# Kernel optimization log

Hardware: AMD Instinct MI355X
Metric: run time of the kernel (lower is better)

## Reference

```python
import jax, jax.numpy as jnp
import numpy as np
from jax import lax

ALPHA = 50.0
BN_EPS = 1e-5
L2_EPS = 1e-12

N, C, H, W = 32, 128, 128, 128
K = 64  # num_clusters


def _l2norm(v, axis):
    n = jnp.sqrt(jnp.sum(v * v, axis=axis, keepdims=True))
    return v / jnp.maximum(n, L2_EPS)


def setup_inputs() -> dict:
    key = jax.random.key(0)
    ks = jax.random.split(key, 4)
    x = jax.random.normal(ks[0], (N, C, H, W), dtype=jnp.float32)
    conv_w = jax.random.normal(ks[1], (C, C, 3, 3), dtype=jnp.float32) * 0.05
    bn_gamma = jnp.ones((C,), jnp.float32)
    bn_beta = jnp.zeros((C,), jnp.float32)
    bn_mean = jnp.zeros((C,), jnp.float32)
    bn_var = jnp.ones((C,), jnp.float32)
    # conv.weight in NetVLAD is centroids.permute(1,0): shape (dim, num_clusters)
    vlad_w = jax.random.normal(ks[2], (C, K), dtype=jnp.float32)
    vlad_b = jnp.zeros((K,), jnp.float32)  # initialized to zeros in _init_params
    return {"input": x, "conv_w": conv_w, "bn_gamma": bn_gamma, "bn_beta": bn_beta,
            "bn_mean": bn_mean, "bn_var": bn_var, "vlad_w": vlad_w, "vlad_b": vlad_b,
            "norm_flag": 1}


def reference(input, conv_w, bn_gamma, bn_beta, bn_mean, bn_var, vlad_w, vlad_b, norm_flag):
    # bottleneck_layer_2: conv3x3 stride2 pad1 (no bias) -> BN (eval form) -> ReLU
    f = lax.conv_general_dilated(input, conv_w, window_strides=(2, 2),
                                 padding=[(1, 1), (1, 1)],
                                 dimension_numbers=("NCHW", "OIHW", "NCHW"))
    inv = bn_gamma / jnp.sqrt(bn_var + BN_EPS)
    f = f * inv[None, :, None, None] + (bn_beta - bn_mean * inv)[None, :, None, None]
    f = jax.nn.relu(f)

    n, c, h, w = f.shape
    hw = h * w
    # normalize_input: L2 over channel dim
    xn = _l2norm(f, axis=1)
    xf = xn.reshape(n, c, hw)  # (N,C,HW)

    # soft assignment: x^T @ normalize(W, dim=0), bias added, softmax over clusters
    wn = _l2norm(vlad_w, axis=0)                     # (C,K)
    sa_ = jnp.einsum("nci,ck->nik", xf, wn)          # (N,HW,K)
    logits = jnp.swapaxes(sa_, 1, 2) + vlad_b[None, :, None]  # (N,K,HW)
    a = jax.nn.softmax(ALPHA * logits, axis=1)       # softmax over K

    # vlad_k = sum_i a_ki * x_i - (sum_i a_ki) * c_k  (c_k = vlad_w[:,k], unnormalized)
    asum = jnp.sum(a, axis=-1)                       # (N,K)
    vlad = jnp.einsum("nki,nci->nkc", a, xf) - asum[:, :, None] * vlad_w.T[None]  # (N,K,C)

    vlad = _l2norm(vlad, axis=2)                     # intra-normalization
    vlad = vlad.reshape(n, -1)
    vlad = _l2norm(vlad, axis=1)

    feature = jnp.swapaxes(xf, 1, 2)                 # (N,HW,C)
    soft_assign_out = jnp.swapaxes(sa_, 1, 2)        # (N,K,HW)
    return (vlad, soft_assign_out, feature)
```

## Files before the change

### kernel.cpp

```cpp
#include <hip/hip_runtime.h>

typedef short short8 __attribute__((ext_vector_type(8)));
typedef float floatx4 __attribute__((ext_vector_type(4)));

#define ALPHA 50.0f
#define BN_EPS 1e-5f

#define SA_BASE   262144L
#define FEAT_BASE 8650752L

#define T_OFF    0L
#define AW_OFF   0L
#define XNT_OFF  138444800L
#define WB_OFF   171999232L
#define WNA_OFF  172294144L
#define ASUM_OFF 172310528L

__device__ __forceinline__ unsigned short f2bf(float f) {
    unsigned u = __builtin_bit_cast(unsigned, f);
    u = u + 0x7FFFu + ((u >> 16) & 1u);
    return (unsigned short)(u >> 16);
}

__global__ __launch_bounds__(256) void k_prep(const float* __restrict__ conv_w,
                                              const float* __restrict__ vlad_w,
                                              unsigned short* __restrict__ wB,
                                              unsigned short* __restrict__ wnA,
                                              float* __restrict__ asum) {
    int b = blockIdx.x, t = threadIdx.x;
    if (b < 576) {
        int idx = b * 256 + t;
        int ci = idx & 127, co = (idx >> 7) & 127, tap = idx >> 14;
        float w = conv_w[(co * 128 + ci) * 9 + tap];
        wB[(tap * 128 + co) * 128 + ci] = f2bf(w);
    } else {
        if (t < 64) {
            int k = t;
            float s = 0.0f;
            for (int c = 0; c < 128; c++) { float w = vlad_w[c * 64 + k]; s += w * w; }
            float rs = 1.0f / fmaxf(sqrtf(s), 1e-12f);
            for (int c = 0; c < 128; c++) wnA[k * 128 + c] = f2bf(vlad_w[c * 64 + k] * rs);
        } else {
            for (int i = t - 64; i < 2048; i += 192) asum[i] = 0.0f;
        }
    }
}

__global__ __launch_bounds__(256) void k_border(unsigned short* __restrict__ T) {
    int n = blockIdx.x, t = threadIdx.x;
    uint4 z = make_uint4(0, 0, 0, 0);
    for (int i = t; i < 4128; i += 256) {
        long e;
        if (i < 2080) {
            int ix = i >> 4, oct = i & 15;
            e = (((long)n * 130 + 0) * 130 + ix) * 128 + oct * 8;
        } else {
            int j = i - 2080;
            int row = (j >> 4) + 1, oct = j & 15;
            e = (((long)n * 130 + row) * 130 + 0) * 128 + oct * 8;
        }
        *(uint4*)(T + e) = z;
    }
}

__global__ __launch_bounds__(256) void k_xform(const float* __restrict__ in,
                                               unsigned short* __restrict__ T) {
    int y = blockIdx.x, n = blockIdx.y, t = threadIdx.x;
    __shared__ float ls[32 * 132];
    for (int cc = 0; cc < 4; cc++) {
        __syncthreads();
        int ci0 = cc * 32;
        for (int i = 0; i < 4; i++) {
            int idx = i * 256 + t;
            int ci = idx >> 5, xq = idx & 31;
            float4 v = *(const float4*)(in + ((((long)n * 128 + ci0 + ci) * 128 + y) * 128 + xq * 4));
            *(float4*)(&ls[ci * 132 + xq * 4]) = v;
        }
        __syncthreads();
        int x = t >> 1, half = t & 1;
        for (int o = 0; o < 2; o++) {
            short8 pk;
#pragma unroll
            for (int j = 0; j < 8; j++) {
                int lci = half * 16 + o * 8 + j;
                pk[j] = (short)f2bf(ls[lci * 132 + x]);
            }
            long e = (((long)n * 130 + y + 1) * 130 + (x + 1)) * 128 + ci0 + half * 16 + o * 8;
            *(short8*)(T + e) = pk;
        }
    }
}

__global__ __launch_bounds__(256) void k_conv(const unsigned short* __restrict__ T,
                                              const unsigned short* __restrict__ wB,
                                              const float* __restrict__ gamma,
                                              const float* __restrict__ beta,
                                              const float* __restrict__ mean,
                                              const float* __restrict__ var,
                                              float* __restrict__ out,
                                              unsigned short* __restrict__ xnT) {
    int ypair = blockIdx.x, n = blockIdx.y;
    int t = threadIdx.x, lane = t & 63, w = t >> 6;
    int wm = w >> 1, wn = w & 1;
    int s = lane & 15, q = lane >> 4;
    int y0 = ypair * 2;

    __shared__ short lsA[26000];
    __shared__ float lsq[256];

    floatx4 acc[4][4];
#pragma unroll
    for (int a = 0; a < 4; a++)
#pragma unroll
        for (int b = 0; b < 4; b++) acc[a][b] = (floatx4){0.f, 0.f, 0.f, 0.f};

    const unsigned short* Tbase = T + (((long)n * 130 + 2 * y0) * 130) * 128;

    int abase0 = 10400 * wm + q * 8;
    int bbase0 = (wn * 64 + s) * 128 + q * 8;

    for (int cc = 0; cc < 4; cc++) {
        int ci0 = cc * 32;
        for (int i = 0; i < 11; i++) {
            int idx = i * 256 + t;
            if (idx < 2600) {
                int oct = idx & 3, rem = idx >> 2;
                int ix = rem % 130, r = rem / 130;
                uint4 v = *(const uint4*)(Tbase + (long)(r * 130 + ix) * 128 + ci0 + oct * 8);
                *(uint4*)(&lsA[(r * 130 + ix) * 40 + oct * 8]) = v;
            }
        }
        __syncthreads();
#pragma unroll
        for (int tap = 0; tap < 9; tap++) {
            int dy = tap / 3, dx = tap % 3;
            short8 af[4], bf[4];
#pragma unroll
            for (int tm = 0; tm < 4; tm++) {
                int x = tm * 16 + s;
                af[tm] = *(const short8*)(&lsA[abase0 + 80 * x + 5200 * dy + 40 * dx]);
            }
#pragma unroll
            for (int tn = 0; tn < 4; tn++) {
                bf[tn] = *(const short8*)(wB + bbase0 + tap * 16384 + tn * 2048 + ci0);
            }
#pragma unroll
            for (int tm = 0; tm < 4; tm++)
#pragma unroll
                for (int tn = 0; tn < 4; tn++)
                    acc[tm][tn] = __builtin_amdgcn_mfma_f32_16x16x32_bf16(af[tm], bf[tn], acc[tm][tn], 0, 0, 0);
        }
        __syncthreads();
    }

    float inv[4], bt[4];
#pragma unroll
    for (int tn = 0; tn < 4; tn++) {
        int co = wn * 64 + tn * 16 + s;
        inv[tn] = gamma[co] / sqrtf(var[co] + BN_EPS);
        bt[tn] = beta[co] - mean[co] * inv[tn];
    }
#pragma unroll
    for (int tm = 0; tm < 4; tm++)
#pragma unroll
        for (int tn = 0; tn < 4; tn++)
#pragma unroll
            for (int r = 0; r < 4; r++) {
                float f = acc[tm][tn][r] * inv[tn] + bt[tn];
                acc[tm][tn][r] = fmaxf(f, 0.0f);
            }
#pragma unroll
    for (int tm = 0; tm < 4; tm++)
#pragma unroll
        for (int r = 0; r < 4; r++) {
            float p = 0.f;
#pragma unroll
            for (int tn = 0; tn < 4; tn++) { float f = acc[tm][tn][r]; p += f * f; }
            p += __shfl_xor(p, 1); p += __shfl_xor(p, 2);
            p += __shfl_xor(p, 4); p += __shfl_xor(p, 8);
            if (s == 0) lsq[wn * 128 + wm * 64 + tm * 16 + q * 4 + r] = p;
        }
    __syncthreads();
    float scl[4][4];
#pragma unroll
    for (int tm = 0; tm < 4; tm++)
#pragma unroll
        for (int r = 0; r < 4; r++) {
            int m = wm * 64 + tm * 16 + q * 4 + r;
            float tot = lsq[m] + lsq[128 + m];
            scl[tm][r] = 1.0f / fmaxf(sqrtf(tot), 1e-12f);
        }
    short* lsT = lsA;
    long pixbase = (long)n * 4096 + y0 * 64;
#pragma unroll
    for (int tm = 0; tm < 4; tm++)
#pragma unroll
        for (int r = 0; r < 4; r++) {
            int m = wm * 64 + tm * 16 + q * 4 + r;
#pragma unroll
            for (int tn = 0; tn < 4; tn++) {
                int co = wn * 64 + tn * 16 + s;
                float xv = acc[tm][tn][r] * scl[tm][r];
                out[FEAT_BASE + (pixbase + m) * 128 + co] = xv;
                lsT[co * 136 + m] = (short)f2bf(xv);
            }
        }
    __syncthreads();
    {
        int co = t >> 1, mh = t & 1;
        long base = ((long)n * 128 + co) * 4096 + y0 * 64 + mh * 64;
#pragma unroll
        for (int o = 0; o < 8; o++) {
            short8 v = *(short8*)(&lsT[co * 136 + mh * 64 + o * 8]);
            *(short8*)(xnT + base + o * 8) = v;
        }
    }
}

__global__ __launch_bounds__(256) void k_sa(const float* __restrict__ feat,
                                            const unsigned short* __restrict__ wnA,
                                            const float* __restrict__ vlad_b,
                                            float* __restrict__ out,
                                            unsigned short* __restrict__ aout,
                                            float* __restrict__ asum) {
    int pt = blockIdx.x, n = blockIdx.y;
    int t = threadIdx.x, lane = t & 63, w = t >> 6;
    int s = lane & 15, q = lane >> 4;
    int pb = pt * 256 + w * 64;

    floatx4 acc[4][4];
#pragma unroll
    for (int a = 0; a < 4; a++)
#pragma unroll
        for (int b = 0; b < 4; b++) acc[a][b] = (floatx4){0.f, 0.f, 0.f, 0.f};

    const float* fb = feat + FEAT_BASE + (long)n * 4096 * 128;
#pragma unroll
    for (int kk = 0; kk < 4; kk++) {
        int c0 = kk * 32 + q * 8;
        short8 af[4], bf[4];
#pragma unroll
        for (int tm = 0; tm < 4; tm++)
            af[tm] = *(const short8*)(wnA + (tm * 16 + s) * 128 + c0);
#pragma unroll
        for (int tn = 0; tn < 4; tn++) {
            const float* p = fb + (long)(pb + tn * 16 + s) * 128 + c0;
            float4 v0 = *(const float4*)p;
            float4 v1 = *(const float4*)(p + 4);
            short8 bv;
            bv[0] = (short)f2bf(v0.x); bv[1] = (short)f2bf(v0.y);
            bv[2] = (short)f2bf(v0.z); bv[3] = (short)f2bf(v0.w);
            bv[4] = (short)f2bf(v1.x); bv[5] = (short)f2bf(v1.y);
            bv[6] = (short)f2bf(v1.z); bv[7] = (short)f2bf(v1.w);
            bf[tn] = bv;
        }
#pragma unroll
        for (int tm = 0; tm < 4; tm++)
#pragma unroll
            for (int tn = 0; tn < 4; tn++)
                acc[tm][tn] = __builtin_amdgcn_mfma_f32_16x16x32_bf16(af[tm], bf[tn], acc[tm][tn], 0, 0, 0);
    }
    long sabase = SA_BASE + (long)n * 64 * 4096;
#pragma unroll
    for (int tm = 0; tm < 4; tm++)
#pragma unroll
        for (int r = 0; r < 4; r++) {
            int k = tm * 16 + q * 4 + r;
#pragma unroll
            for (int tn = 0; tn < 4; tn++)
                out[sabase + (long)k * 4096 + pb + tn * 16 + s] = acc[tm][tn][r];
        }
    float bv[4][4];
#pragma unroll
    for (int tm = 0; tm < 4; tm++)
#pragma unroll
        for (int r = 0; r < 4; r++) bv[tm][r] = vlad_b[tm * 16 + q * 4 + r];
#pragma unroll
    for (int tn = 0; tn < 4; tn++) {
        float M = -1e30f;
#pragma unroll
        for (int tm = 0; tm < 4; tm++)
#pragma unroll
            for (int r = 0; r < 4; r++)
                M = fmaxf(M, ALPHA * (acc[tm][tn][r] + bv[tm][r]));
        M = fmaxf(M, __shfl_xor(M, 16)); M = fmaxf(M, __shfl_xor(M, 32));
        float S = 0.f;
#pragma unroll
        for (int tm = 0; tm < 4; tm++)
#pragma unroll
            for (int r = 0; r < 4; r++) {
                float p = expf(ALPHA * (acc[tm][tn][r] + bv[tm][r]) - M);
                acc[tm][tn][r] = p; S += p;
            }
        S += __shfl_xor(S, 16); S += __shfl_xor(S, 32);
        float rS = 1.0f / S;
#pragma unroll
        for (int tm = 0; tm < 4; tm++)
#pragma unroll
            for (int r = 0; r < 4; r++) acc[tm][tn][r] *= rS;
    }
    long abase = (long)n * 64 * 4096;
#pragma unroll
    for (int tm = 0; tm < 4; tm++)
#pragma unroll
        for (int r = 0; r < 4; r++) {
            int k = tm * 16 + q * 4 + r;
#pragma unroll
            for (int tn = 0; tn < 4; tn++)
                aout[abase + (long)k * 4096 + pb + tn * 16 + s] = f2bf(acc[tm][tn][r]);
            float p = acc[tm][0][r] + acc[tm][1][r] + acc[tm][2][r] + acc[tm][3][r];
            p += __shfl_xor(p, 1); p += __shfl_xor(p, 2);
            p += __shfl_xor(p, 4); p += __shfl_xor(p, 8);
            if (s == 0) atomicAdd(asum + n * 64 + k, p);
        }
}

__global__ __launch_bounds__(256) void k_vlad(const unsigned short* __restrict__ aw,
                                              const unsigned short* __restrict__ xnT,
                                              const float* __restrict__ vlad_w,
                                              const float* __restrict__ asum,
                                              float* __restrict__ out) {
    int n = blockIdx.x;
    int t = threadIdx.x, lane = t & 63, w = t >> 6;
    int wm = w >> 1, wn = w & 1;
    int s = lane & 15, q = lane >> 4;

    floatx4 acc[2][4];
#pragma unroll
    for (int a = 0; a < 2; a++)
#pragma unroll
        for (int b = 0; b < 4; b++) acc[a][b] = (floatx4){0.f, 0.f, 0.f, 0.f};

    const unsigned short* ab = aw + (long)n * 64 * 4096;
    const unsigned short* xb = xnT + (long)n * 128 * 4096;
    for (int i0 = 0; i0 < 4096; i0 += 32) {
        short8 af[2], bf[4];
#pragma unroll
        for (int tm = 0; tm < 2; tm++)
            af[tm] = *(const short8*)(ab + (long)(wm * 32 + tm * 16 + s) * 4096 + i0 + q * 8);
#pragma unroll
        for (int tn = 0; tn < 4; tn++)
            bf[tn] = *(const short8*)(xb + (long)(wn * 64 + tn * 16 + s) * 4096 + i0 + q * 8);
#pragma unroll
        for (int tm = 0; tm < 2; tm++)
#pragma unroll
            for (int tn = 0; tn < 4; tn++)
                acc[tm][tn] = __builtin_amdgcn_mfma_f32_16x16x32_bf16(af[tm], bf[tn], acc[tm][tn], 0, 0, 0);
    }
    __shared__ float lsq[128];
    __shared__ float gsq[4];
#pragma unroll
    for (int tm = 0; tm < 2; tm++)
#pragma unroll
        for (int r = 0; r < 4; r++) {
            int k = wm * 32 + tm * 16 + q * 4 + r;
            float as = asum[n * 64 + k];
#pragma unroll
            for (int tn = 0; tn < 4; tn++) {
                int c = wn * 64 + tn * 16 + s;
                acc[tm][tn][r] -= as * vlad_w[c * 64 + k];
            }
        }
#pragma unroll
    for (int tm = 0; tm < 2; tm++)
#pragma unroll
        for (int r = 0; r < 4; r++) {
            float p = 0.f;
#pragma unroll
            for (int tn = 0; tn < 4; tn++) { float f = acc[tm][tn][r]; p += f * f; }
            p += __shfl_xor(p, 1); p += __shfl_xor(p, 2);
            p += __shfl_xor(p, 4); p += __shfl_xor(p, 8);
            if (s == 0) lsq[wn * 64 + wm * 32 + tm * 16 + q * 4 + r] = p;
        }
    __syncthreads();
#pragma unroll
    for (int tm = 0; tm < 2; tm++)
#pragma unroll
        for (int r = 0; r < 4; r++) {
            int k = wm * 32 + tm * 16 + q * 4 + r;
            float tot = lsq[k] + lsq[64 + k];
            float sc = 1.0f / fmaxf(sqrtf(tot), 1e-12f);
#pragma unroll
            for (int tn = 0; tn < 4; tn++) acc[tm][tn][r] *= sc;
        }
    float ps = 0.f;
#pragma unroll
    for (int tm = 0; tm < 2; tm++)
#pragma unroll
        for (int tn = 0; tn < 4; tn++)
#pragma unroll
            for (int r = 0; r < 4; r++) { float f = acc[tm][tn][r]; ps += f * f; }
    ps += __shfl_xor(ps, 1); ps += __shfl_xor(ps, 2); ps += __shfl_xor(ps, 4);
    ps += __shfl_xor(ps, 8); ps += __shfl_xor(ps, 16); ps += __shfl_xor(ps, 32);
    if (lane == 0) gsq[w] = ps;
    __syncthreads();
    float tot = gsq[0] + gsq[1] + gsq[2] + gsq[3];
    float sc2 = 1.0f / fmaxf(sqrtf(tot), 1e-12f);
#pragma unroll
    for (int tm = 0; tm < 2; tm++)
#pragma unroll
        for (int r = 0; r < 4; r++) {
            int k = wm * 32 + tm * 16 + q * 4 + r;
#pragma unroll
            for (int tn = 0; tn < 4; tn++) {
                int c = wn * 64 + tn * 16 + s;
                out[((long)n * 64 + k) * 128 + c] = acc[tm][tn][r] * sc2;
            }
        }
}

extern "C" void kernel_launch(void* const* d_in, const int* in_sizes, int n_in,
                              void* d_out, int out_size, void* d_ws, size_t ws_size,
                              hipStream_t stream) {
    const float* input  = (const float*)d_in[0];
    const float* conv_w = (const float*)d_in[1];
    const float* gamma  = (const float*)d_in[2];
    const float* beta   = (const float*)d_in[3];
    const float* mean   = (const float*)d_in[4];
    const float* var    = (const float*)d_in[5];
    const float* vlad_w = (const float*)d_in[6];
    const float* vlad_b = (const float*)d_in[7];
    float* out = (float*)d_out;
    char* ws = (char*)d_ws;

    unsigned short* T   = (unsigned short*)(ws + T_OFF);
    unsigned short* aw  = (unsigned short*)(ws + AW_OFF);
    unsigned short* xnT = (unsigned short*)(ws + XNT_OFF);
    unsigned short* wB  = (unsigned short*)(ws + WB_OFF);
    unsigned short* wnA = (unsigned short*)(ws + WNA_OFF);
    float* asum         = (float*)(ws + ASUM_OFF);

    k_prep<<<577, 256, 0, stream>>>(conv_w, vlad_w, wB, wnA, asum);
    k_border<<<32, 256, 0, stream>>>(T);
    k_xform<<<dim3(128, 32), 256, 0, stream>>>(input, T);
    k_conv<<<dim3(32, 32), 256, 0, stream>>>(T, wB, gamma, beta, mean, var, out, xnT);
    k_sa<<<dim3(16, 32), 256, 0, stream>>>(out, wnA, vlad_b, out, aw, asum);
    k_vlad<<<32, 256, 0, stream>>>(aw, xnT, vlad_w, asum, out);
}
```

Measured before the change: 715.7 us.

## Split VLAD reduction across blocks, async LDS loads in conv, wider xform tiles

The VLAD aggregation kernel, which previously ran only 32 blocks, is split into a 16-way chunked partial-sum kernel plus a small reduction/normalization kernel, so the GEMM runs on far more CUs. The conv kernel's input staging now uses global_load_lds with an XOR-swizzled, unpadded LDS layout to cut register traffic and bank conflicts. The transpose kernel stages 64 channels at a time with an odd row pitch to avoid LDS bank conflicts. The cost is an extra launch and a partial-sum buffer written to and read from global memory.

```diff
diff --git a/kernel.cpp b/kernel.cpp
--- a/kernel.cpp
+++ b/kernel.cpp
@@ -11,6 +11,7 @@
 
 #define T_OFF    0L
 #define AW_OFF   0L
+#define PART_OFF 50331648L
 #define XNT_OFF  138444800L
 #define WB_OFF   171999232L
 #define WNA_OFF  172294144L
@@ -20,6 +21,12 @@
     unsigned u = __builtin_bit_cast(unsigned, f);
     u = u + 0x7FFFu + ((u >> 16) & 1u);
     return (unsigned short)(u >> 16);
+}
+
+__device__ __forceinline__ void gl_lds16(const void* g, void* l) {
+    __builtin_amdgcn_global_load_lds(
+        (const __attribute__((address_space(1))) unsigned int*)g,
+        (__attribute__((address_space(3))) unsigned int*)l, 16, 0, 0);
 }
 
 __global__ __launch_bounds__(256) void k_prep(const float* __restrict__ conv_w,
@@ -66,26 +73,27 @@
 __global__ __launch_bounds__(256) void k_xform(const float* __restrict__ in,
                                                unsigned short* __restrict__ T) {
     int y = blockIdx.x, n = blockIdx.y, t = threadIdx.x;
-    __shared__ float ls[32 * 132];
-    for (int cc = 0; cc < 4; cc++) {
+    __shared__ float ls[64 * 133];
+    for (int cc = 0; cc < 2; cc++) {
         __syncthreads();
-        int ci0 = cc * 32;
-        for (int i = 0; i < 4; i++) {
+        int ci0 = cc * 64;
+#pragma unroll
+        for (int i = 0; i < 8; i++) {
             int idx = i * 256 + t;
             int ci = idx >> 5, xq = idx & 31;
             float4 v = *(const float4*)(in + ((((long)n * 128 + ci0 + ci) * 128 + y) * 128 + xq * 4));
-            *(float4*)(&ls[ci * 132 + xq * 4]) = v;
+            *(float4*)(&ls[ci * 133 + xq * 4]) = v;
         }
         __syncthreads();
-        int x = t >> 1, half = t & 1;
-        for (int o = 0; o < 2; o++) {
+#pragma unroll
+        for (int i = 0; i < 4; i++) {
+            int idx = i * 256 + t;
+            int x = idx >> 3, oct = idx & 7;
             short8 pk;
 #pragma unroll
-            for (int j = 0; j < 8; j++) {
-                int lci = half * 16 + o * 8 + j;
-                pk[j] = (short)f2bf(ls[lci * 132 + x]);
-            }
-            long e = (((long)n * 130 + y + 1) * 130 + (x + 1)) * 128 + ci0 + half * 16 + o * 8;
+            for (int j = 0; j < 8; j++)
+                pk[j] = (short)f2bf(ls[(oct * 8 + j) * 133 + x]);
+            long e = (((long)n * 130 + y + 1) * 130 + (x + 1)) * 128 + ci0 + oct * 8;
             *(short8*)(T + e) = pk;
         }
     }
@@ -105,7 +113,7 @@
     int s = lane & 15, q = lane >> 4;
     int y0 = ypair * 2;
 
-    __shared__ short lsA[26000];
+    __shared__ __align__(16) short lsA[20800];
     __shared__ float lsq[256];
 
     floatx4 acc[4][4];
@@ -115,35 +123,41 @@
         for (int b = 0; b < 4; b++) acc[a][b] = (floatx4){0.f, 0.f, 0.f, 0.f};
 
     const unsigned short* Tbase = T + (((long)n * 130 + 2 * y0) * 130) * 128;
-
-    int abase0 = 10400 * wm + q * 8;
     int bbase0 = (wn * 64 + s) * 128 + q * 8;
 
     for (int cc = 0; cc < 4; cc++) {
         int ci0 = cc * 32;
+        const unsigned short* Tc = Tbase + ci0;
+#pragma unroll
         for (int i = 0; i < 11; i++) {
-            int idx = i * 256 + t;
-            if (idx < 2600) {
-                int oct = idx & 3, rem = idx >> 2;
-                int ix = rem % 130, r = rem / 130;
-                uint4 v = *(const uint4*)(Tbase + (long)(r * 130 + ix) * 128 + ci0 + oct * 8);
-                *(uint4*)(&lsA[(r * 130 + ix) * 40 + oct * 8]) = v;
+            int f = i * 256 + t;
+            short* lbase = &lsA[2048 * i + 512 * w];
+            if (f < 2600) {
+                int r = f / 520;
+                int rem = f - r * 520;
+                int p = rem >> 3;
+                int o8 = (rem & 7) ^ (p & 7);
+                int ix = 2 * p + (o8 >> 2);
+                int oct = o8 & 3;
+                gl_lds16(Tc + (((long)(r * 130 + ix)) << 7) + (oct << 3), lbase);
             }
         }
         __syncthreads();
 #pragma unroll
         for (int tap = 0; tap < 9; tap++) {
-            int dy = tap / 3, dx = tap % 3;
+            const int dy = tap / 3, dx = tap % 3;
             short8 af[4], bf[4];
 #pragma unroll
             for (int tm = 0; tm < 4; tm++) {
                 int x = tm * 16 + s;
-                af[tm] = *(const short8*)(&lsA[abase0 + 80 * x + 5200 * dy + 40 * dx]);
-            }
-#pragma unroll
-            for (int tn = 0; tn < 4; tn++) {
+                int p = x + (dx >> 1);
+                int o8p = (((dx & 1) << 2) | q) ^ (p & 7);
+                int r = 2 * wm + dy;
+                af[tm] = *(const short8*)(&lsA[(((r * 65 + p) << 3) + o8p) << 3]);
+            }
+#pragma unroll
+            for (int tn = 0; tn < 4; tn++)
                 bf[tn] = *(const short8*)(wB + bbase0 + tap * 16384 + tn * 2048 + ci0);
-            }
 #pragma unroll
             for (int tm = 0; tm < 4; tm++)
 #pragma unroll
@@ -315,12 +329,10 @@
         }
 }
 
-__global__ __launch_bounds__(256) void k_vlad(const unsigned short* __restrict__ aw,
-                                              const unsigned short* __restrict__ xnT,
-                                              const float* __restrict__ vlad_w,
-                                              const float* __restrict__ asum,
-                                              float* __restrict__ out) {
-    int n = blockIdx.x;
+__global__ __launch_bounds__(256) void k_vlad1(const unsigned short* __restrict__ aw,
+                                               const unsigned short* __restrict__ xnT,
+                                               float* __restrict__ part) {
+    int ch = blockIdx.x, n = blockIdx.y;
     int t = threadIdx.x, lane = t & 63, w = t >> 6;
     int wm = w >> 1, wn = w & 1;
     int s = lane & 15, q = lane >> 4;
@@ -333,7 +345,8 @@
 
     const unsigned short* ab = aw + (long)n * 64 * 4096;
     const unsigned short* xb = xnT + (long)n * 128 * 4096;
-    for (int i0 = 0; i0 < 4096; i0 += 32) {
+    int ibeg = ch * 256, iend = ibeg + 256;
+    for (int i0 = ibeg; i0 < iend; i0 += 32) {
         short8 af[2], bf[4];
 #pragma unroll
         for (int tm = 0; tm < 2; tm++)
@@ -347,66 +360,62 @@
             for (int tn = 0; tn < 4; tn++)
                 acc[tm][tn] = __builtin_amdgcn_mfma_f32_16x16x32_bf16(af[tm], bf[tn], acc[tm][tn], 0, 0, 0);
     }
+    float* pb = part + ((long)n * 16 + ch) * 8192;
+#pragma unroll
+    for (int tm = 0; tm < 2; tm++)
+#pragma unroll
+        for (int r = 0; r < 4; r++) {
+            int k = wm * 32 + tm * 16 + q * 4 + r;
+#pragma unroll
+            for (int tn = 0; tn < 4; tn++) {
+                int c = wn * 64 + tn * 16 + s;
+                pb[k * 128 + c] = acc[tm][tn][r];
+            }
+        }
+}
+
+__global__ __launch_bounds__(256) void k_vlad2(const float* __restrict__ part,
+                                               const float* __restrict__ vlad_w,
+                                               const float* __restrict__ asum,
+                                               float* __restrict__ out) {
+    int n = blockIdx.x;
+    int t = threadIdx.x, lane = t & 63, w = t >> 6;
     __shared__ float lsq[128];
     __shared__ float gsq[4];
-#pragma unroll
-    for (int tm = 0; tm < 2; tm++)
-#pragma unroll
-        for (int r = 0; r < 4; r++) {
-            int k = wm * 32 + tm * 16 + q * 4 + r;
-            float as = asum[n * 64 + k];
-#pragma unroll
-            for (int tn = 0; tn < 4; tn++) {
-                int c = wn * 64 + tn * 16 + s;
-                acc[tm][tn][r] -= as * vlad_w[c * 64 + k];
-            }
-        }
-#pragma unroll
-    for (int tm = 0; tm < 2; tm++)
-#pragma unroll
-        for (int r = 0; r < 4; r++) {
-            float p = 0.f;
-#pragma unroll
-            for (int tn = 0; tn < 4; tn++) { float f = acc[tm][tn][r]; p += f * f; }
-            p += __shfl_xor(p, 1); p += __shfl_xor(p, 2);
-            p += __shfl_xor(p, 4); p += __shfl_xor(p, 8);
-            if (s == 0) lsq[wn * 64 + wm * 32 + tm * 16 + q * 4 + r] = p;
-        }
+
+    float v[32];
+    const float* pb = part + (long)n * 16 * 8192;
+#pragma unroll
+    for (int j = 0; j < 32; j++) {
+        int e = j * 256 + t;
+        float sacc = 0.f;
+#pragma unroll
+        for (int c8 = 0; c8 < 16; c8++) sacc += pb[c8 * 8192 + e];
+        int k = e >> 7, c = e & 127;
+        sacc -= asum[n * 64 + k] * vlad_w[c * 64 + k];
+        v[j] = sacc;
+        float p = sacc * sacc;
+        p += __shfl_xor(p, 1); p += __shfl_xor(p, 2); p += __shfl_xor(p, 4);
+        p += __shfl_xor(p, 8); p += __shfl_xor(p, 16); p += __shfl_xor(p, 32);
+        if (lane == 0) lsq[j * 4 + w] = p;
+    }
     __syncthreads();
-#pragma unroll
-    for (int tm = 0; tm < 2; tm++)
-#pragma unroll
-        for (int r = 0; r < 4; r++) {
-            int k = wm * 32 + tm * 16 + q * 4 + r;
-            float tot = lsq[k] + lsq[64 + k];
-            float sc = 1.0f / fmaxf(sqrtf(tot), 1e-12f);
-#pragma unroll
-            for (int tn = 0; tn < 4; tn++) acc[tm][tn][r] *= sc;
-        }
-    float ps = 0.f;
-#pragma unroll
-    for (int tm = 0; tm < 2; tm++)
-#pragma unroll
-        for (int tn = 0; tn < 4; tn++)
-#pragma unroll
-            for (int r = 0; r < 4; r++) { float f = acc[tm][tn][r]; ps += f * f; }
-    ps += __shfl_xor(ps, 1); ps += __shfl_xor(ps, 2); ps += __shfl_xor(ps, 4);
-    ps += __shfl_xor(ps, 8); ps += __shfl_xor(ps, 16); ps += __shfl_xor(ps, 32);
-    if (lane == 0) gsq[w] = ps;
+    float gp = 0.f;
+#pragma unroll
+    for (int j = 0; j < 32; j++) {
+        float tot = lsq[j * 4 + (w & 2)] + lsq[j * 4 + (w & 2) + 1];
+        float sc = 1.0f / fmaxf(sqrtf(tot), 1e-12f);
+        v[j] *= sc;
+        gp += v[j] * v[j];
+    }
+    gp += __shfl_xor(gp, 1); gp += __shfl_xor(gp, 2); gp += __shfl_xor(gp, 4);
+    gp += __shfl_xor(gp, 8); gp += __shfl_xor(gp, 16); gp += __shfl_xor(gp, 32);
+    if (lane == 0) gsq[w] = gp;
     __syncthreads();
-    float tot = gsq[0] + gsq[1] + gsq[2] + gsq[3];
-    float sc2 = 1.0f / fmaxf(sqrtf(tot), 1e-12f);
-#pragma unroll
-    for (int tm = 0; tm < 2; tm++)
-#pragma unroll
-        for (int r = 0; r < 4; r++) {
-            int k = wm * 32 + tm * 16 + q * 4 + r;
-#pragma unroll
-            for (int tn = 0; tn < 4; tn++) {
-                int c = wn * 64 + tn * 16 + s;
-                out[((long)n * 64 + k) * 128 + c] = acc[tm][tn][r] * sc2;
-            }
-        }
+    float sc2 = 1.0f / fmaxf(sqrtf(gsq[0] + gsq[1] + gsq[2] + gsq[3]), 1e-12f);
+#pragma unroll
+    for (int j = 0; j < 32; j++)
+        out[(long)n * 8192 + j * 256 + t] = v[j] * sc2;
 }
 
 extern "C" void kernel_launch(void* const* d_in, const int* in_sizes, int n_in,
@@ -425,6 +434,7 @@
 
     unsigned short* T   = (unsigned short*)(ws + T_OFF);
     unsigned short* aw  = (unsigned short*)(ws + AW_OFF);
+    float* part         = (float*)(ws + PART_OFF);
     unsigned short* xnT = (unsigned short*)(ws + XNT_OFF);
     unsigned short* wB  = (unsigned short*)(ws + WB_OFF);
     unsigned short* wnA = (unsigned short*)(ws + WNA_OFF);
@@ -435,5 +445,6 @@
     k_xform<<<dim3(128, 32), 256, 0, stream>>>(input, T);
     k_conv<<<dim3(32, 32), 256, 0, stream>>>(T, wB, gamma, beta, mean, var, out, xnT);
     k_sa<<<dim3(16, 32), 256, 0, stream>>>(out, wnA, vlad_b, out, aw, asum);
-    k_vlad<<<32, 256, 0, stream>>>(aw, xnT, vlad_w, asum, out);
-}
+    k_vlad1<<<dim3(16, 32), 256, 0, stream>>>(aw, xnT, part);
+    k_vlad2<<<32, 256, 0, stream>>>(part, vlad_w, asum, out);
+}
```

Result: faster. 610.0 us (-14.8%).
